# Kernel tuning notes

Measured on AMD Instinct MI355X. Metric: run time of the kernel, lower is better.

Reference implementation:

```python
import jax, jax.numpy as jnp
import numpy as np

IN_FEATURES = 4096
OUT_FEATURES = 4096


def setup_inputs() -> dict:
    key = jax.random.key(0)
    k1, k2 = jax.random.split(key)
    x = jax.random.normal(k1, (4, 2048, IN_FEATURES), dtype=jnp.float32)
    latent_weight = jax.random.normal(k2, (OUT_FEATURES, IN_FEATURES), dtype=jnp.float32) * 0.02
    return {"x": x, "latent_weight": latent_weight}


def _quantize(w):
    # abs-mean scale, ternary {-alpha, 0, alpha} with threshold 0.5*alpha
    alpha = jnp.mean(jnp.abs(w))
    threshold = 0.5 * alpha
    return jnp.where(w > threshold, alpha, jnp.where(w < -threshold, -alpha, jnp.zeros_like(w)))


def reference(x, latent_weight):
    qw = _quantize(latent_weight.astype(jnp.float32))
    # F.linear: x @ qw.T  -> [B, S, out_features]
    out = jnp.einsum('bsi,oi->bso', x.astype(jnp.float32), qw)
    return out.astype(x.dtype)
```

## Files before the change

kernel.cpp:

```cpp
#include <hip/hip_runtime.h>
#include <hip/hip_bf16.h>
#include <stdint.h>

#define M_DIM 8192
#define K_DIM 4096
#define N_DIM 4096

typedef __attribute__((ext_vector_type(8))) short short8;
typedef __attribute__((ext_vector_type(4))) float f32x4;

__device__ __forceinline__ void lds_load16(const ushort* g, ushort* l) {
    __builtin_amdgcn_global_load_lds(
        (const __attribute__((address_space(1))) uint32_t*)g,
        (__attribute__((address_space(3))) uint32_t*)l, 16, 0, 0);
}

__device__ __forceinline__ ushort f2bf_rne(float f) {
    uint32_t u = __float_as_uint(f);
    uint32_t r = (u + 0x7FFFu + ((u >> 16) & 1u)) >> 16;
    return (ushort)r;
}

__global__ void k_abs_partial(const float* __restrict__ w, double* __restrict__ partial) {
    const float4* w4 = (const float4*)w;
    const int n4 = (K_DIM * N_DIM) / 4;
    double s = 0.0;
    for (int i = blockIdx.x * blockDim.x + threadIdx.x; i < n4; i += gridDim.x * blockDim.x) {
        float4 v = w4[i];
        s += (double)fabsf(v.x) + (double)fabsf(v.y) + (double)fabsf(v.z) + (double)fabsf(v.w);
    }
    #pragma unroll
    for (int off = 32; off > 0; off >>= 1) s += __shfl_down(s, off, 64);
    __shared__ double sm[4];
    int lane = threadIdx.x & 63, wv = threadIdx.x >> 6;
    if (lane == 0) sm[wv] = s;
    __syncthreads();
    if (threadIdx.x == 0) partial[blockIdx.x] = sm[0] + sm[1] + sm[2] + sm[3];
}

__global__ void k_alpha(const double* __restrict__ partial, float* __restrict__ alpha_out) {
    double s = 0.0;
    for (int i = threadIdx.x; i < 1024; i += 256) s += partial[i];
    #pragma unroll
    for (int off = 32; off > 0; off >>= 1) s += __shfl_down(s, off, 64);
    __shared__ double sm[4];
    int lane = threadIdx.x & 63, wv = threadIdx.x >> 6;
    if (lane == 0) sm[wv] = s;
    __syncthreads();
    if (threadIdx.x == 0) {
        double total = sm[0] + sm[1] + sm[2] + sm[3];
        alpha_out[0] = (float)(total * (1.0 / 16777216.0));
    }
}

__global__ void k_quant(const float* __restrict__ w, const float* __restrict__ alpha_p,
                        ushort* __restrict__ qw) {
    const float thr = 0.5f * alpha_p[0];
    int i = blockIdx.x * blockDim.x + threadIdx.x;
    float4 v = ((const float4*)w)[i];
    ushort4 q;
    q.x = v.x > thr ? 0x3F80 : (v.x < -thr ? 0xBF80 : 0);
    q.y = v.y > thr ? 0x3F80 : (v.y < -thr ? 0xBF80 : 0);
    q.z = v.z > thr ? 0x3F80 : (v.z < -thr ? 0xBF80 : 0);
    q.w = v.w > thr ? 0x3F80 : (v.w < -thr ? 0xBF80 : 0);
    ((ushort4*)qw)[i] = q;
}

__global__ void k_cast(const float* __restrict__ x, ushort* __restrict__ xb) {
    int i = blockIdx.x * blockDim.x + threadIdx.x;
    float4 v = ((const float4*)x)[i];
    ushort4 o;
    o.x = f2bf_rne(v.x);
    o.y = f2bf_rne(v.y);
    o.z = f2bf_rne(v.z);
    o.w = f2bf_rne(v.w);
    ((ushort4*)xb)[i] = o;
}

#define BM 128
#define BN 128
#define BK 64

__global__ __launch_bounds__(256, 2) void k_gemm(const ushort* __restrict__ A,
                                                 const ushort* __restrict__ B,
                                                 const float* __restrict__ alpha_p,
                                                 float* __restrict__ C) {
    __shared__ __align__(16) ushort sA[BM * BK];
    __shared__ __align__(16) ushort sB[BN * BK];

    const int tid = threadIdx.x;
    const int lane = tid & 63;
    const int bm = blockIdx.y, bn = blockIdx.x;
    const int wv = tid >> 6;
    const int wm = (wv & 1) * 64;
    const int wn = (wv >> 1) * 64;

    f32x4 acc[4][4] = {};

    const ushort* Abase = A + (size_t)(bm * BM) * K_DIM;
    const ushort* Bbase = B + (size_t)(bn * BN) * K_DIM;

    const int r = lane & 15, q = lane >> 4;

    for (int kb = 0; kb < K_DIM / BK; ++kb) {
        const int k0 = kb * BK;
        #pragma unroll
        for (int j = 0; j < 4; ++j) {
            int c = j * 256 + tid;
            int row = c >> 3, kc = (c & 7) * 8;
            lds_load16(Abase + (size_t)row * K_DIM + k0 + kc, &sA[c * 8]);
            lds_load16(Bbase + (size_t)row * K_DIM + k0 + kc, &sB[c * 8]);
        }
        __syncthreads();

        #pragma unroll
        for (int kk = 0; kk < BK; kk += 32) {
            short8 af[4], bfr[4];
            #pragma unroll
            for (int i = 0; i < 4; ++i)
                af[i] = *(const short8*)&sA[(wm + i * 16 + r) * BK + kk + q * 8];
            #pragma unroll
            for (int j = 0; j < 4; ++j)
                bfr[j] = *(const short8*)&sB[(wn + j * 16 + r) * BK + kk + q * 8];
            #pragma unroll
            for (int i = 0; i < 4; ++i)
                #pragma unroll
                for (int j = 0; j < 4; ++j)
                    acc[i][j] = __builtin_amdgcn_mfma_f32_16x16x32_bf16(af[i], bfr[j], acc[i][j], 0, 0, 0);
        }
        __syncthreads();
    }

    const float alpha = alpha_p[0];
    #pragma unroll
    for (int i = 0; i < 4; ++i)
        #pragma unroll
        for (int j = 0; j < 4; ++j)
            #pragma unroll
            for (int v = 0; v < 4; ++v) {
                int row = bm * BM + wm + i * 16 + q * 4 + v;
                int col = bn * BN + wn + j * 16 + r;
                C[(size_t)row * N_DIM + col] = alpha * acc[i][j][v];
            }
}

extern "C" void kernel_launch(void* const* d_in, const int* in_sizes, int n_in,
                              void* d_out, int out_size, void* d_ws, size_t ws_size,
                              hipStream_t stream) {
    const float* x = (const float*)d_in[0];
    const float* w = (const float*)d_in[1];
    float* out = (float*)d_out;

    char* ws = (char*)d_ws;
    double* partial = (double*)ws;
    float* alpha = (float*)(ws + 8192);
    ushort* qw = (ushort*)(ws + 16384);
    ushort* xb = (ushort*)(ws + 16384 + (size_t)K_DIM * N_DIM * 2);

    k_abs_partial<<<1024, 256, 0, stream>>>(w, partial);
    k_alpha<<<1, 256, 0, stream>>>(partial, alpha);
    k_quant<<<(K_DIM * N_DIM / 4) / 256, 256, 0, stream>>>(w, alpha, qw);
    k_cast<<<(M_DIM * K_DIM / 4) / 256, 256, 0, stream>>>(x, xb);

    dim3 grid(N_DIM / BN, M_DIM / BM);
    k_gemm<<<grid, dim3(256), 0, stream>>>(xb, qw, alpha, out);
}
```

Measured before the change: 550.9 us.

## Swizzle GEMM LDS layout and fuse x cast into abs-sum prep kernel

The GEMM now applies an XOR swizzle on the 16-byte k-chunk index when staging A and B tiles into LDS, and on the fragment reads, to cut LDS bank conflicts on the MFMA operand loads. Separately, the weight abs-sum reduction and the fp32-to-bf16 cast of x are merged into one kernel launch using disjoint block ranges, so the two memory-bound passes can run concurrently and one launch is dropped. The swizzle adds a little index arithmetic per load.

Measured after the change: 553.1 us. No clear change (+0.4%).

```diff
diff --git a/kernel.cpp b/kernel.cpp
--- a/kernel.cpp
+++ b/kernel.cpp
@@ -21,21 +21,40 @@
     return (ushort)r;
 }
 
-__global__ void k_abs_partial(const float* __restrict__ w, double* __restrict__ partial) {
-    const float4* w4 = (const float4*)w;
-    const int n4 = (K_DIM * N_DIM) / 4;
-    double s = 0.0;
-    for (int i = blockIdx.x * blockDim.x + threadIdx.x; i < n4; i += gridDim.x * blockDim.x) {
-        float4 v = w4[i];
-        s += (double)fabsf(v.x) + (double)fabsf(v.y) + (double)fabsf(v.z) + (double)fabsf(v.w);
+__global__ void k_prep(const float* __restrict__ w, double* __restrict__ partial,
+                       const float* __restrict__ x, ushort* __restrict__ xb) {
+    const int tid = threadIdx.x;
+    if (blockIdx.x < 1024) {
+        const float4* w4 = (const float4*)w;
+        const int n4 = (K_DIM * N_DIM) / 4;
+        double s = 0.0;
+        for (int i = blockIdx.x * 256 + tid; i < n4; i += 1024 * 256) {
+            float4 v = w4[i];
+            s += (double)fabsf(v.x) + (double)fabsf(v.y) + (double)fabsf(v.z) + (double)fabsf(v.w);
+        }
+        #pragma unroll
+        for (int off = 32; off > 0; off >>= 1) s += __shfl_down(s, off, 64);
+        __shared__ double sm[4];
+        int lane = tid & 63, wv = tid >> 6;
+        if (lane == 0) sm[wv] = s;
+        __syncthreads();
+        if (tid == 0) partial[blockIdx.x] = sm[0] + sm[1] + sm[2] + sm[3];
+    } else {
+        const int b2 = blockIdx.x - 1024;
+        const float4* x4 = (const float4*)x;
+        ushort4* o4 = (ushort4*)xb;
+        #pragma unroll
+        for (int it = 0; it < 16; ++it) {
+            int i = it * (2048 * 256) + b2 * 256 + tid;
+            float4 v = x4[i];
+            ushort4 o;
+            o.x = f2bf_rne(v.x);
+            o.y = f2bf_rne(v.y);
+            o.z = f2bf_rne(v.z);
+            o.w = f2bf_rne(v.w);
+            o4[i] = o;
+        }
     }
-    #pragma unroll
-    for (int off = 32; off > 0; off >>= 1) s += __shfl_down(s, off, 64);
-    __shared__ double sm[4];
-    int lane = threadIdx.x & 63, wv = threadIdx.x >> 6;
-    if (lane == 0) sm[wv] = s;
-    __syncthreads();
-    if (threadIdx.x == 0) partial[blockIdx.x] = sm[0] + sm[1] + sm[2] + sm[3];
 }
 
 __global__ void k_alpha(const double* __restrict__ partial, float* __restrict__ alpha_out) {
@@ -66,17 +85,6 @@
     ((ushort4*)qw)[i] = q;
 }
 
-__global__ void k_cast(const float* __restrict__ x, ushort* __restrict__ xb) {
-    int i = blockIdx.x * blockDim.x + threadIdx.x;
-    float4 v = ((const float4*)x)[i];
-    ushort4 o;
-    o.x = f2bf_rne(v.x);
-    o.y = f2bf_rne(v.y);
-    o.z = f2bf_rne(v.z);
-    o.w = f2bf_rne(v.w);
-    ((ushort4*)xb)[i] = o;
-}
-
 #define BM 128
 #define BN 128
 #define BK 64
@@ -102,14 +110,23 @@
 
     const int r = lane & 15, q = lane >> 4;
 
+    int srow[4], skc[4];
+    #pragma unroll
+    for (int j = 0; j < 4; ++j) {
+        int c = j * 256 + tid;
+        int row = c >> 3;
+        int k8 = (c & 7) ^ (row & 7);
+        srow[j] = row;
+        skc[j] = k8 * 8;
+    }
+
     for (int kb = 0; kb < K_DIM / BK; ++kb) {
         const int k0 = kb * BK;
         #pragma unroll
         for (int j = 0; j < 4; ++j) {
             int c = j * 256 + tid;
-            int row = c >> 3, kc = (c & 7) * 8;
-            lds_load16(Abase + (size_t)row * K_DIM + k0 + kc, &sA[c * 8]);
-            lds_load16(Bbase + (size_t)row * K_DIM + k0 + kc, &sB[c * 8]);
+            lds_load16(Abase + (size_t)srow[j] * K_DIM + k0 + skc[j], &sA[c * 8]);
+            lds_load16(Bbase + (size_t)srow[j] * K_DIM + k0 + skc[j], &sB[c * 8]);
         }
         __syncthreads();
 
@@ -117,11 +134,17 @@
         for (int kk = 0; kk < BK; kk += 32) {
             short8 af[4], bfr[4];
             #pragma unroll
-            for (int i = 0; i < 4; ++i)
-                af[i] = *(const short8*)&sA[(wm + i * 16 + r) * BK + kk + q * 8];
+            for (int i = 0; i < 4; ++i) {
+                int ra = wm + i * 16 + r;
+                int pos = ((kk >> 3) + q) ^ (ra & 7);
+                af[i] = *(const short8*)&sA[ra * BK + pos * 8];
+            }
             #pragma unroll
-            for (int j = 0; j < 4; ++j)
-                bfr[j] = *(const short8*)&sB[(wn + j * 16 + r) * BK + kk + q * 8];
+            for (int j = 0; j < 4; ++j) {
+                int rb = wn + j * 16 + r;
+                int pos = ((kk >> 3) + q) ^ (rb & 7);
+                bfr[j] = *(const short8*)&sB[rb * BK + pos * 8];
+            }
             #pragma unroll
             for (int i = 0; i < 4; ++i)
                 #pragma unroll
@@ -157,10 +180,9 @@
     ushort* qw = (ushort*)(ws + 16384);
     ushort* xb = (ushort*)(ws + 16384 + (size_t)K_DIM * N_DIM * 2);
 
-    k_abs_partial<<<1024, 256, 0, stream>>>(w, partial);
+    k_prep<<<3072, 256, 0, stream>>>(w, partial, x, xb);
     k_alpha<<<1, 256, 0, stream>>>(partial, alpha);
     k_quant<<<(K_DIM * N_DIM / 4) / 256, 256, 0, stream>>>(w, alpha, qw);
-    k_cast<<<(M_DIM * K_DIM / 4) / 256, 256, 0, stream>>>(x, xb);
 
     dim3 grid(N_DIM / BN, M_DIM / BM);
     k_gemm<<<grid, dim3(256), 0, stream>>>(xb, qw, alpha, out);
```
